# Kernel optimization log

Measured on AMD Instinct MI355X. Metric: run time of the kernel, lower is better.

## Reference

```python
import jax, jax.numpy as jnp
import numpy as np

HIDDEN = 2048
N_HEADS = 16
N_KV = 8
HEAD_DIM = HIDDEN // N_HEADS  # 128
EPS = 1e-6


def rms_norm(x, w, eps=EPS):
    xf = x.astype(jnp.float32)
    var = jnp.mean(xf * xf, axis=-1, keepdims=True)
    return (w * (xf * jax.lax.rsqrt(var + eps)).astype(x.dtype))


def rotate_half(x):
    x1, x2 = jnp.split(x, 2, axis=-1)
    return jnp.concatenate([-x2, x1], axis=-1)


def setup_inputs() -> dict:
    key = jax.random.key(0)
    ks = jax.random.split(key, 8)
    B, S = 2, 2048
    inp = {
        "hidden_states": jax.random.normal(ks[0], (B, S, HIDDEN), jnp.float32),
        "cos": jax.random.uniform(ks[1], (B, S, HEAD_DIM), jnp.float32, -1.0, 1.0),
        "sin": jax.random.uniform(ks[2], (B, S, HEAD_DIM), jnp.float32, -1.0, 1.0),
        "Wq": jax.random.normal(ks[3], (N_HEADS * HEAD_DIM, HIDDEN), jnp.float32) * 0.02,
        "Wk": jax.random.normal(ks[4], (N_KV * HEAD_DIM, HIDDEN), jnp.float32) * 0.02,
        "Wv": jax.random.normal(ks[5], (N_KV * HEAD_DIM, HIDDEN), jnp.float32) * 0.02,
        "Wo": jax.random.normal(ks[6], (HIDDEN, N_HEADS * HEAD_DIM), jnp.float32) * 0.02,
        "q_norm_w": jnp.ones((HEAD_DIM,), jnp.float32),
        "k_norm_w": jnp.ones((HEAD_DIM,), jnp.float32),
    }
    return inp


def reference(hidden_states, cos, sin, Wq, Wk, Wv, Wo, q_norm_w, k_norm_w):
    B, S, _ = hidden_states.shape
    scale = HEAD_DIM ** -0.5
    n_rep = N_HEADS // N_KV

    q = (hidden_states @ Wq.T).reshape(B, S, N_HEADS, HEAD_DIM)
    k = (hidden_states @ Wk.T).reshape(B, S, N_KV, HEAD_DIM)
    v = (hidden_states @ Wv.T).reshape(B, S, N_KV, HEAD_DIM)

    q = rms_norm(q, q_norm_w)
    k = rms_norm(k, k_norm_w)

    # -> (B, H, S, D)
    q = q.transpose(0, 2, 1, 3)
    k = k.transpose(0, 2, 1, 3)
    v = v.transpose(0, 2, 1, 3)

    c = cos[:, None, :, :]  # (B,1,S,D)
    s = sin[:, None, :, :]
    q = q * c + rotate_half(q) * s
    k = k * c + rotate_half(k) * s

    k = jnp.repeat(k, n_rep, axis=1)
    v = jnp.repeat(v, n_rep, axis=1)

    scores = jnp.einsum("bhqd,bhkd->bhqk", q, k) * scale
    attn = jax.nn.softmax(scores.astype(jnp.float32), axis=-1).astype(hidden_states.dtype)
    out = jnp.einsum("bhqk,bhkd->bhqd", attn, v)
    out = out.transpose(0, 2, 1, 3).reshape(B, S, N_HEADS * HEAD_DIM)
    return out @ Wo.T
```

## Files before the change

### kernel.cpp

```cpp
#include <hip/hip_runtime.h>
#include <cstdint>

#define SEQ 2048
#define BATCH 2
#define TOK 4096
#define HID 2048
#define NH 16
#define NKV 8
#define HD 128
#define QKV_LD 4096

using f16x8 = __attribute__((ext_vector_type(8))) _Float16;
using f32x4 = __attribute__((ext_vector_type(4))) float;

#define MFMA(a, b, c) __builtin_amdgcn_mfma_f32_16x16x32_f16(a, b, c, 0, 0, 0)

__device__ inline void gload16(const void* g, void* l) {
    __builtin_amdgcn_global_load_lds(
        (const __attribute__((address_space(1))) unsigned*)g,
        (__attribute__((address_space(3))) unsigned*)l, 16, 0, 0);
}

__device__ inline float exp2_fast(float x) {
#if __has_builtin(__builtin_amdgcn_exp2f)
    return __builtin_amdgcn_exp2f(x);
#else
    float r;
    asm("v_exp_f32 %0, %1\n\ts_nop 1" : "=v"(r) : "v"(x));
    return r;
#endif
}

__global__ __launch_bounds__(256) void conv_all(
    const float* __restrict__ hidden, const float* __restrict__ Wq,
    const float* __restrict__ Wk, const float* __restrict__ Wv,
    const float* __restrict__ Wo, _Float16* __restrict__ HhG,
    _Float16* __restrict__ WallH, _Float16* __restrict__ WoH)
{
    const int bid = blockIdx.x;
    const float* src;
    _Float16* dst;
    int row;
    if (bid < 4096)      { row = bid;        src = hidden; dst = HhG; }
    else if (bid < 6144) { row = bid - 4096; src = Wq;     dst = WallH; }
    else if (bid < 7168) { row = bid - 6144; src = Wk;     dst = WallH + (size_t)2048 * HID; }
    else if (bid < 8192) { row = bid - 7168; src = Wv;     dst = WallH + (size_t)3072 * HID; }
    else                 { row = bid - 8192; src = Wo;     dst = WoH; }

    const int gch = threadIdx.x;
    const float* s = src + (size_t)row * HID + gch * 8;
    float4 a = *(const float4*)s;
    float4 b = *(const float4*)(s + 4);
    f16x8 v;
    v[0] = (_Float16)a.x; v[1] = (_Float16)a.y;
    v[2] = (_Float16)a.z; v[3] = (_Float16)a.w;
    v[4] = (_Float16)b.x; v[5] = (_Float16)b.y;
    v[6] = (_Float16)b.z; v[7] = (_Float16)b.w;
    *(f16x8*)((char*)dst + (size_t)row * 4096 + gch * 16) = v;
}

template<bool HALF_OUT>
__global__ __launch_bounds__(512, 2) void gemm256(
    const _Float16* __restrict__ Ag, const _Float16* __restrict__ Bg,
    void* __restrict__ Cv, int ldc, int K)
{
    __shared__ char lds[2][4][16384];

    const int tid = threadIdx.x;
    const int wv = tid >> 6, ln = tid & 63;
    const int wm = wv >> 2, wn = wv & 3;
    const int lr = ln & 15, lq = ln >> 4;
    const int bn = blockIdx.x, bm = blockIdx.y;

    f32x4 acc[8][4] = {};

    const size_t arow0 = (size_t)bm * 256;
    const size_t brow0 = (size_t)bn * 256;

    const int g = tid & 7;
    uint32_t offA[2][2], offB[2][2];
#pragma unroll
    for (int i = 0; i < 2; ++i) {
        const int row = (i * 512 + tid) >> 3;
        const uint32_t sw = (uint32_t)((g ^ (row & 7)) << 4);
        offA[0][i] = (uint32_t)((arow0 + row) * 4096) + sw;
        offA[1][i] = (uint32_t)((arow0 + 128 + row) * 4096) + sw;
        offB[0][i] = (uint32_t)((brow0 + row) * 4096) + sw;
        offB[1][i] = (uint32_t)((brow0 + 128 + row) * 4096) + sw;
    }
    const int dst0 = wv * 64 * 16;

    const int swz0 = ((lq ^ (lr & 7)) << 4);
    const int swz1 = (((4 + lq) ^ (lr & 7)) << 4);

#define STAGE_ALL(bufsel, t)                                                   \
    { _Pragma("unroll")                                                        \
      for (int i = 0; i < 2; ++i) {                                            \
        gload16((const char*)Ag + offA[0][i] + (size_t)(t) * 128,              \
                &lds[bufsel][0][i * 8192 + dst0]);                             \
        gload16((const char*)Ag + offA[1][i] + (size_t)(t) * 128,              \
                &lds[bufsel][1][i * 8192 + dst0]);                             \
        gload16((const char*)Bg + offB[0][i] + (size_t)(t) * 128,              \
                &lds[bufsel][2][i * 8192 + dst0]);                             \
        gload16((const char*)Bg + offB[1][i] + (size_t)(t) * 128,              \
                &lds[bufsel][3][i * 8192 + dst0]);                             \
      } }

    STAGE_ALL(0, 0);
    asm volatile("s_waitcnt vmcnt(0)" ::: "memory");
    __builtin_amdgcn_s_barrier();

    const int NT = K / 64;
    for (int t = 0; t < NT; ++t) {
        const int buf = t & 1;
        const char* Ab = &lds[buf][wm][0];
        const char* Bb = &lds[buf][2 + (wn >> 1)][(wn & 1) * 64 * 128];

        f16x8 bfr[4][2];
#pragma unroll
        for (int nj = 0; nj < 4; ++nj) {
            bfr[nj][0] = *(const f16x8*)(Bb + (nj * 16 + lr) * 128 + swz0);
            bfr[nj][1] = *(const f16x8*)(Bb + (nj * 16 + lr) * 128 + swz1);
        }

        if (t + 1 < NT) STAGE_ALL(buf ^ 1, t + 1);

        __builtin_amdgcn_s_setprio(1);
#pragma unroll
        for (int mi = 0; mi < 8; ++mi) {
            f16x8 a0 = *(const f16x8*)(Ab + (mi * 16 + lr) * 128 + swz0);
            f16x8 a1 = *(const f16x8*)(Ab + (mi * 16 + lr) * 128 + swz1);
#pragma unroll
            for (int nj = 0; nj < 4; ++nj) {
                acc[mi][nj] = MFMA(a0, bfr[nj][0], acc[mi][nj]);
                acc[mi][nj] = MFMA(a1, bfr[nj][1], acc[mi][nj]);
            }
        }
        __builtin_amdgcn_s_setprio(0);

        asm volatile("s_waitcnt vmcnt(0)" ::: "memory");
        __builtin_amdgcn_s_barrier();
    }
#undef STAGE_ALL

#pragma unroll
    for (int mi = 0; mi < 8; ++mi)
#pragma unroll
        for (int r = 0; r < 4; ++r) {
            const size_t rowoff =
                (size_t)(arow0 + wm * 128 + mi * 16 + lq * 4 + r) * ldc
                + brow0 + wn * 64 + lr;
            if constexpr (HALF_OUT) {
                _Float16* rowp = (_Float16*)Cv + rowoff;
#pragma unroll
                for (int nj = 0; nj < 4; ++nj)
                    rowp[nj * 16] = (_Float16)acc[mi][nj][r];
            } else {
                float* rowp = (float*)Cv + rowoff;
#pragma unroll
                for (int nj = 0; nj < 4; ++nj)
                    rowp[nj * 16] = acc[mi][nj][r];
            }
        }
}

__global__ __launch_bounds__(512, 1) void gemm256x128(
    const _Float16* __restrict__ Ag, const _Float16* __restrict__ Bg,
    float* __restrict__ C, int ldc, int K)
{
    __shared__ char lds[2][3][16384];

    const int tid = threadIdx.x;
    const int wv = tid >> 6, ln = tid & 63;
    const int wm = wv >> 1, wn = wv & 1;
    const int lr = ln & 15, lq = ln >> 4;
    const int bn = blockIdx.x, bm = blockIdx.y;

    f32x4 acc[4][4] = {};

    const size_t arow0 = (size_t)bm * 256;
    const size_t brow0 = (size_t)bn * 128;

    const int g = tid & 7;
    uint32_t offA[2][2], offB[2];
#pragma unroll
    for (int i = 0; i < 2; ++i) {
        const int row = (i * 512 + tid) >> 3;
        const uint32_t sw = (uint32_t)((g ^ (row & 7)) << 4);
        offA[0][i] = (uint32_t)((arow0 + row) * 4096) + sw;
        offA[1][i] = (uint32_t)((arow0 + 128 + row) * 4096) + sw;
        offB[i]    = (uint32_t)((brow0 + row) * 4096) + sw;
    }
    const int dst0 = wv * 64 * 16;

    const int swz0 = ((lq ^ (lr & 7)) << 4);
    const int swz1 = (((4 + lq) ^ (lr & 7)) << 4);

#define STAGE_ALL2(bufsel, t)                                                  \
    { _Pragma("unroll")                                                        \
      for (int i = 0; i < 2; ++i) {                                            \
        gload16((const char*)Ag + offA[0][i] + (size_t)(t) * 128,              \
                &lds[bufsel][0][i * 8192 + dst0]);                             \
        gload16((const char*)Ag + offA[1][i] + (size_t)(t) * 128,              \
                &lds[bufsel][1][i * 8192 + dst0]);                             \
        gload16((const char*)Bg + offB[i] + (size_t)(t) * 128,                 \
                &lds[bufsel][2][i * 8192 + dst0]);                             \
      } }

    STAGE_ALL2(0, 0);
    asm volatile("s_waitcnt vmcnt(0)" ::: "memory");
    __builtin_amdgcn_s_barrier();

    const int NT = K / 64;
    for (int t = 0; t < NT; ++t) {
        const int buf = t & 1;
        const char* Ab = &lds[buf][wm >> 1][(wm & 1) * 64 * 128];
        const char* Bb = &lds[buf][2][wn * 64 * 128];

        f16x8 bfr[4][2];
#pragma unroll
        for (int nj = 0; nj < 4; ++nj) {
            bfr[nj][0] = *(const f16x8*)(Bb + (nj * 16 + lr) * 128 + swz0);
            bfr[nj][1] = *(const f16x8*)(Bb + (nj * 16 + lr) * 128 + swz1);
        }

        if (t + 1 < NT) STAGE_ALL2(buf ^ 1, t + 1);

        __builtin_amdgcn_s_setprio(1);
#pragma unroll
        for (int mi = 0; mi < 4; ++mi) {
            f16x8 a0 = *(const f16x8*)(Ab + (mi * 16 + lr) * 128 + swz0);
            f16x8 a1 = *(const f16x8*)(Ab + (mi * 16 + lr) * 128 + swz1);
#pragma unroll
            for (int nj = 0; nj < 4; ++nj) {
                acc[mi][nj] = MFMA(a0, bfr[nj][0], acc[mi][nj]);
                acc[mi][nj] = MFMA(a1, bfr[nj][1], acc[mi][nj]);
            }
        }
        __builtin_amdgcn_s_setprio(0);

        asm volatile("s_waitcnt vmcnt(0)" ::: "memory");
        __builtin_amdgcn_s_barrier();
    }
#undef STAGE_ALL2

#pragma unroll
    for (int mi = 0; mi < 4; ++mi)
#pragma unroll
        for (int r = 0; r < 4; ++r) {
            float* rowp = C + (size_t)(arow0 + wm * 64 + mi * 16 + lq * 4 + r) * ldc
                          + brow0 + wn * 64 + lr;
#pragma unroll
            for (int nj = 0; nj < 4; ++nj)
                rowp[nj * 16] = acc[mi][nj][r];
        }
}

__global__ __launch_bounds__(256) void norm_rope(
    const _Float16* __restrict__ P, const float* __restrict__ cosb,
    const float* __restrict__ sinb, const float* __restrict__ qw,
    const float* __restrict__ kw, _Float16* __restrict__ QhG,
    _Float16* __restrict__ KhG)
{
    const int t    = blockIdx.y;
    const int wave = threadIdx.x >> 6;
    const int lane = threadIdx.x & 63;
    const int hid  = blockIdx.x * 4 + wave;
    const float QS = 0.08838834764831845f * 1.4426950408889634f;

    const _Float16* ptr;
    const float* w;
    if (hid < NH) { ptr = P + (size_t)t * QKV_LD + hid * HD;              w = qw; }
    else          { ptr = P + (size_t)t * QKV_LD + HID + (hid - NH) * HD; w = kw; }

    float x1 = (float)ptr[lane];
    float x2 = (float)ptr[lane + 64];
    float ss = x1 * x1 + x2 * x2;
#pragma unroll
    for (int off = 1; off < 64; off <<= 1) ss += __shfl_xor(ss, off);
    const float r = rsqrtf(ss * (1.f / 128.f) + 1e-6f);
    const float n1 = x1 * r * w[lane];
    const float n2 = x2 * r * w[lane + 64];

    const float* cp = cosb + (size_t)t * HD;
    const float* sp = sinb + (size_t)t * HD;
    const float o1 = n1 * cp[lane]      - n2 * sp[lane];
    const float o2 = n2 * cp[lane + 64] + n1 * sp[lane + 64];

    if (hid < NH) {
        _Float16* qrow = QhG + (size_t)t * HID + hid * HD;
        qrow[lane]      = (_Float16)(o1 * QS);
        qrow[lane + 64] = (_Float16)(o2 * QS);
    } else {
        const int b = t / SEQ, s = t % SEQ, kv = hid - NH;
        char* ph = (char*)KhG + ((size_t)(b * NKV + kv) * SEQ + s) * 256;
        const int s7 = s & 7;
        const int d1 = lane, d2 = lane + 64;
        *(_Float16*)(ph + (((d1 >> 3) ^ s7) << 4) + ((d1 & 7) << 1)) = (_Float16)o1;
        *(_Float16*)(ph + (((d2 >> 3) ^ s7) << 4) + ((d2 & 7) << 1)) = (_Float16)o2;
    }
}

__global__ __launch_bounds__(256) void conv_v(
    const _Float16* __restrict__ P, _Float16* __restrict__ VtG)
{
    __shared__ _Float16 Ts[64][136];
    const int kb = blockIdx.x;
    const int kv = blockIdx.y;
    const int tid = threadIdx.x;

#pragma unroll
    for (int r = 0; r < 4; ++r) {
        const int idx = tid + r * 256;
        const int row = idx >> 4, c8 = idx & 15;
        *(f16x8*)&Ts[row][c8 * 8] =
            *(const f16x8*)(P + (size_t)(kb * 64 + row) * QKV_LD
                            + HID + NKV * HD + kv * HD + c8 * 8);
    }
    __syncthreads();

    const int b  = (kb * 64) / SEQ;
    const int s0 = (kb * 64) % SEQ;
#pragma unroll
    for (int w = 0; w < 4; ++w) {
        const int idx = tid + w * 256;
        const int d = idx >> 3, c = idx & 7;
        f16x8 pk;
#pragma unroll
        for (int kk = 0; kk < 8; ++kk) pk[kk] = Ts[c * 8 + kk][d];
        char* dst = (char*)VtG + ((size_t)(b * NKV + kv) * 128 + d) * 4096
                    + ((s0 >> 3) + (c ^ (d & 7))) * 16;
        *(f16x8*)dst = pk;
    }
}

__global__ __launch_bounds__(256, 2) void flash_f16(
    const _Float16* __restrict__ QhG, const _Float16* __restrict__ KhG,
    const _Float16* __restrict__ VtG, _Float16* __restrict__ OH)
{
    __shared__ char KhL[2][16384];
    __shared__ char VtL[16384];
    __shared__ _Float16 Pl[4][32][72];

    const int id  = blockIdx.x + 16 * (blockIdx.y + 16 * blockIdx.z);
    const int swz = (id & 7) * 64 + (id >> 3);
    const int qt = swz & 15, h = (swz >> 4) & 15, b = swz >> 8;

    const int hkv = h >> 1;
    const int tid = threadIdx.x, wv = tid >> 6, ln = tid & 63;
    const int lr = ln & 15, lq = ln >> 4;
    const int qbase = qt * 128 + wv * 32;
    const float BIAS = 3.0f * 1.4426950408889634f;

    f16x8 qh[2][4];
#pragma unroll
    for (int mi = 0; mi < 2; ++mi)
#pragma unroll
        for (int kc = 0; kc < 4; ++kc)
            qh[mi][kc] = *(const f16x8*)(QhG
                + (size_t)(b * SEQ + qbase + mi * 16 + lr) * HID
                + h * HD + kc * 32 + lq * 8);

    f32x4 o_[2][8] = {};
    float rs[2][4] = {};

    const size_t krow = (size_t)(b * NKV + hkv) * SEQ;
    const size_t vrow = (size_t)(b * NKV + hkv) * 128;

    const char* kg[4];
    const char* vg[4];
    int dofs[4];
#pragma unroll
    for (int r = 0; r < 4; ++r) {
        const int idx = tid + r * 256;
        kg[r] = (const char*)KhG + (krow + (idx >> 4)) * 256 + (idx & 15) * 16;
        vg[r] = (const char*)VtG + (vrow + (idx >> 3)) * 4096 + (idx & 7) * 16;
        dofs[r] = (r * 256 + wv * 64) * 16;
    }

#define STAGE_K(buf, kt)                                                      \
    { _Pragma("unroll")                                                       \
      for (int r = 0; r < 4; ++r)                                             \
          gload16(kg[r] + (size_t)(kt) * 16384, &KhL[buf][dofs[r]]); }
#define STAGE_V(kt)                                                           \
    { _Pragma("unroll")                                                       \
      for (int r = 0; r < 4; ++r)                                             \
          gload16(vg[r] + (kt) * 128, &VtL[dofs[r]]); }

    STAGE_K(0, 0);
    STAGE_V(0);
    STAGE_K(1, 1);
    __syncthreads();

    const int NT = SEQ / 64;
    for (int kt = 0; kt < NT; ++kt) {
        const int buf = kt & 1;

        f32x4 s[2][4];
        __builtin_amdgcn_s_setprio(1);
#pragma unroll
        for (int nt = 0; nt < 4; ++nt) {
            const int key = nt * 16 + lr;
            f16x8 kh[4];
#pragma unroll
            for (int kc = 0; kc < 4; ++kc)
                kh[kc] = *(f16x8*)(&KhL[buf][key * 256 +
                                   ((((kc * 4 + lq) ^ (lr & 7))) << 4)]);
#pragma unroll
            for (int mi = 0; mi < 2; ++mi) {
                f32x4 sa = {-BIAS, -BIAS, -BIAS, -BIAS};
#pragma unroll
                for (int kc = 0; kc < 4; ++kc)
                    sa = MFMA(qh[mi][kc], kh[kc], sa);
                s[mi][nt] = sa;
            }
        }
        __builtin_amdgcn_s_setprio(0);

#pragma unroll
        for (int mi = 0; mi < 2; ++mi)
#pragma unroll
            for (int nt = 0; nt < 4; ++nt)
#pragma unroll
                for (int r = 0; r < 4; ++r) {
                    const float p = exp2_fast(s[mi][nt][r]);
                    rs[mi][r] += p;
                    Pl[wv][mi * 16 + lq * 4 + r][nt * 16 + lr] = (_Float16)p;
                }
        f16x8 pa[2][2];
#pragma unroll
        for (int mi = 0; mi < 2; ++mi) {
            pa[mi][0] = *(f16x8*)&Pl[wv][mi * 16 + lr][lq * 8];
            pa[mi][1] = *(f16x8*)&Pl[wv][mi * 16 + lr][32 + lq * 8];
        }

        if (kt + 1 < NT) {
            asm volatile("s_waitcnt vmcnt(4)" ::: "memory");
        } else {
            asm volatile("s_waitcnt vmcnt(0)" ::: "memory");
        }
        __builtin_amdgcn_s_barrier();

        __builtin_amdgcn_s_setprio(1);
#pragma unroll
        for (int nt2 = 0; nt2 < 8; ++nt2) {
            const int d0 = nt2 * 16 + lr;
            f16x8 v0 = *(f16x8*)(&VtL[d0 * 128 + ((lq ^ (d0 & 7)) << 4)]);
            f16x8 v1 = *(f16x8*)(&VtL[d0 * 128 + (((4 + lq) ^ (d0 & 7)) << 4)]);
#pragma unroll
            for (int mi = 0; mi < 2; ++mi) {
                o_[mi][nt2] = MFMA(pa[mi][0], v0, o_[mi][nt2]);
                o_[mi][nt2] = MFMA(pa[mi][1], v1, o_[mi][nt2]);
            }
        }
        __builtin_amdgcn_s_setprio(0);

        __syncthreads();

        if (kt + 1 < NT) STAGE_V(kt + 1);
        if (kt + 2 < NT) STAGE_K(buf, kt + 2);
    }

    float inv[2][4];
#pragma unroll
    for (int mi = 0; mi < 2; ++mi)
#pragma unroll
        for (int r = 0; r < 4; ++r) {
            float v = rs[mi][r];
            v += __shfl_xor(v, 1);
            v += __shfl_xor(v, 2);
            v += __shfl_xor(v, 4);
            v += __shfl_xor(v, 8);
            inv[mi][r] = 1.0f / v;
        }

#pragma unroll
    for (int mi = 0; mi < 2; ++mi)
#pragma unroll
        for (int r = 0; r < 4; ++r) {
            const int R = b * SEQ + qbase + mi * 16 + lq * 4 + r;
            _Float16* rowp = OH + (size_t)R * HID + h * HD + lr;
#pragma unroll
            for (int nt2 = 0; nt2 < 8; ++nt2)
                rowp[nt2 * 16] = (_Float16)(o_[mi][nt2][r] * inv[mi][r]);
        }
#undef STAGE_K
#undef STAGE_V
}

extern "C" void kernel_launch(void* const* d_in, const int* in_sizes, int n_in,
                              void* d_out, int out_size, void* d_ws, size_t ws_size,
                              hipStream_t stream)
{
    (void)in_sizes; (void)n_in; (void)out_size; (void)ws_size;
    const float* hidden = (const float*)d_in[0];
    const float* cosb   = (const float*)d_in[1];
    const float* sinb   = (const float*)d_in[2];
    const float* Wq     = (const float*)d_in[3];
    const float* Wk     = (const float*)d_in[4];
    const float* Wv     = (const float*)d_in[5];
    const float* Wo     = (const float*)d_in[6];
    const float* qw     = (const float*)d_in[7];
    const float* kw     = (const float*)d_in[8];
    float* out = (float*)d_out;

    char* ws = (char*)d_ws;
    const size_t MB = 1ull << 20;
    _Float16*  P16   = (_Float16*)(ws);
    _Float16*  attnH = (_Float16*)(ws + 32  * MB);
    _Float16*  HhG   = (_Float16*)(ws + 48  * MB);
    _Float16*  WallH = (_Float16*)(ws + 64  * MB);
    _Float16*  WoH   = (_Float16*)(ws + 80  * MB);
    _Float16*  KhG   = (_Float16*)(ws + 88  * MB);
    _Float16*  VtG   = (_Float16*)(ws + 96  * MB);
    _Float16*  QhG   = (_Float16*)(ws + 104 * MB);

    const dim3 blk(256);
    conv_all<<<10240, blk, 0, stream>>>(hidden, Wq, Wk, Wv, Wo, HhG, WallH, WoH);

    gemm256<true><<<dim3(16, 16), dim3(512), 0, stream>>>(HhG, WallH, P16, QKV_LD, HID);

    norm_rope<<<dim3(6, TOK), blk, 0, stream>>>(P16, cosb, sinb, qw, kw, QhG, KhG);
    conv_v<<<dim3(TOK / 64, NKV), blk, 0, stream>>>(P16, VtG);

    flash_f16<<<dim3(SEQ / 128, NH, BATCH), blk, 0, stream>>>(QhG, KhG, VtG, attnH);

    gemm256x128<<<dim3(16, 16), dim3(512), 0, stream>>>(attnH, WoH, out, HID, HID);
}
```

Measured before the change: 215.3 us.

## Double flash-attention query tile per block and remap grid for KV-head locality

Each wave now handles 64 query rows instead of 32, so a block covers 256 queries and each K/V tile loaded into LDS is reused across twice as many rows. The grid is flattened to 256 blocks with an XCD-aware mapping that places both query heads sharing a KV head, and neighbouring query tiles, on the same XCD for L2 reuse. K and V fragments are hoisted into registers before the MFMA loops. The cost is much higher register pressure (launch bounds lowered to 1 block per SM), fewer blocks in total, and lower occupancy for hiding latency.

```diff
diff --git a/kernel.cpp b/kernel.cpp
--- a/kernel.cpp
+++ b/kernel.cpp
@@ -334,35 +334,38 @@
     }
 }
 
-__global__ __launch_bounds__(256, 2) void flash_f16(
+__global__ __launch_bounds__(256, 1) void flash_f16(
     const _Float16* __restrict__ QhG, const _Float16* __restrict__ KhG,
     const _Float16* __restrict__ VtG, _Float16* __restrict__ OH)
 {
     __shared__ char KhL[2][16384];
     __shared__ char VtL[16384];
-    __shared__ _Float16 Pl[4][32][72];
-
-    const int id  = blockIdx.x + 16 * (blockIdx.y + 16 * blockIdx.z);
-    const int swz = (id & 7) * 64 + (id >> 3);
-    const int qt = swz & 15, h = (swz >> 4) & 15, b = swz >> 8;
-
-    const int hkv = h >> 1;
+    __shared__ _Float16 Pl[4][64][72];
+
+    const int raw = blockIdx.x;
+    const int xcd = raw & 7, slot = raw >> 3;
+    const int panel = xcd * 2 + (slot >> 4);
+    const int j = slot & 15;
+    const int b = panel >> 3, hkv = panel & 7;
+    const int h = hkv * 2 + (j & 1);
+    const int qt = j >> 1;
+
     const int tid = threadIdx.x, wv = tid >> 6, ln = tid & 63;
     const int lr = ln & 15, lq = ln >> 4;
-    const int qbase = qt * 128 + wv * 32;
+    const int qbase = qt * 256 + wv * 64;
     const float BIAS = 3.0f * 1.4426950408889634f;
 
-    f16x8 qh[2][4];
-#pragma unroll
-    for (int mi = 0; mi < 2; ++mi)
+    f16x8 qh[4][4];
+#pragma unroll
+    for (int mi = 0; mi < 4; ++mi)
 #pragma unroll
         for (int kc = 0; kc < 4; ++kc)
             qh[mi][kc] = *(const f16x8*)(QhG
                 + (size_t)(b * SEQ + qbase + mi * 16 + lr) * HID
                 + h * HD + kc * 32 + lq * 8);
 
-    f32x4 o_[2][8] = {};
-    float rs[2][4] = {};
+    f32x4 o_[4][8] = {};
+    float rs[4][4] = {};
 
     const size_t krow = (size_t)(b * NKV + hkv) * SEQ;
     const size_t vrow = (size_t)(b * NKV + hkv) * 128;
@@ -396,43 +399,36 @@
     for (int kt = 0; kt < NT; ++kt) {
         const int buf = kt & 1;
 
-        f32x4 s[2][4];
+        f16x8 kh[4][4];
+#pragma unroll
+        for (int nt = 0; nt < 4; ++nt)
+#pragma unroll
+            for (int kc = 0; kc < 4; ++kc)
+                kh[nt][kc] = *(f16x8*)(&KhL[buf][(nt * 16 + lr) * 256 +
+                                       ((((kc * 4 + lq) ^ (lr & 7))) << 4)]);
+
         __builtin_amdgcn_s_setprio(1);
 #pragma unroll
-        for (int nt = 0; nt < 4; ++nt) {
-            const int key = nt * 16 + lr;
-            f16x8 kh[4];
-#pragma unroll
-            for (int kc = 0; kc < 4; ++kc)
-                kh[kc] = *(f16x8*)(&KhL[buf][key * 256 +
-                                   ((((kc * 4 + lq) ^ (lr & 7))) << 4)]);
-#pragma unroll
-            for (int mi = 0; mi < 2; ++mi) {
+        for (int mi = 0; mi < 4; ++mi) {
+            f32x4 s[4];
+#pragma unroll
+            for (int nt = 0; nt < 4; ++nt) {
                 f32x4 sa = {-BIAS, -BIAS, -BIAS, -BIAS};
 #pragma unroll
                 for (int kc = 0; kc < 4; ++kc)
-                    sa = MFMA(qh[mi][kc], kh[kc], sa);
-                s[mi][nt] = sa;
+                    sa = MFMA(qh[mi][kc], kh[nt][kc], sa);
+                s[nt] = sa;
             }
-        }
-        __builtin_amdgcn_s_setprio(0);
-
-#pragma unroll
-        for (int mi = 0; mi < 2; ++mi)
 #pragma unroll
             for (int nt = 0; nt < 4; ++nt)
 #pragma unroll
                 for (int r = 0; r < 4; ++r) {
-                    const float p = exp2_fast(s[mi][nt][r]);
+                    const float p = exp2_fast(s[nt][r]);
                     rs[mi][r] += p;
                     Pl[wv][mi * 16 + lq * 4 + r][nt * 16 + lr] = (_Float16)p;
                 }
-        f16x8 pa[2][2];
-#pragma unroll
-        for (int mi = 0; mi < 2; ++mi) {
-            pa[mi][0] = *(f16x8*)&Pl[wv][mi * 16 + lr][lq * 8];
-            pa[mi][1] = *(f16x8*)&Pl[wv][mi * 16 + lr][32 + lq * 8];
-        }
+        }
+        __builtin_amdgcn_s_setprio(0);
 
         if (kt + 1 < NT) {
             asm volatile("s_waitcnt vmcnt(4)" ::: "memory");
@@ -441,18 +437,28 @@
         }
         __builtin_amdgcn_s_barrier();
 
-        __builtin_amdgcn_s_setprio(1);
+        f16x8 vf[8][2];
 #pragma unroll
         for (int nt2 = 0; nt2 < 8; ++nt2) {
             const int d0 = nt2 * 16 + lr;
-            f16x8 v0 = *(f16x8*)(&VtL[d0 * 128 + ((lq ^ (d0 & 7)) << 4)]);
-            f16x8 v1 = *(f16x8*)(&VtL[d0 * 128 + (((4 + lq) ^ (d0 & 7)) << 4)]);
-#pragma unroll
-            for (int mi = 0; mi < 2; ++mi) {
-                o_[mi][nt2] = MFMA(pa[mi][0], v0, o_[mi][nt2]);
-                o_[mi][nt2] = MFMA(pa[mi][1], v1, o_[mi][nt2]);
+            vf[nt2][0] = *(f16x8*)(&VtL[d0 * 128 + ((lq ^ (d0 & 7)) << 4)]);
+            vf[nt2][1] = *(f16x8*)(&VtL[d0 * 128 + (((4 + lq) ^ (d0 & 7)) << 4)]);
+        }
+        f16x8 pa[4][2];
+#pragma unroll
+        for (int mi = 0; mi < 4; ++mi) {
+            pa[mi][0] = *(f16x8*)&Pl[wv][mi * 16 + lr][lq * 8];
+            pa[mi][1] = *(f16x8*)&Pl[wv][mi * 16 + lr][32 + lq * 8];
+        }
+
+        __builtin_amdgcn_s_setprio(1);
+#pragma unroll
+        for (int nt2 = 0; nt2 < 8; ++nt2)
+#pragma unroll
+            for (int mi = 0; mi < 4; ++mi) {
+                o_[mi][nt2] = MFMA(pa[mi][0], vf[nt2][0], o_[mi][nt2]);
+                o_[mi][nt2] = MFMA(pa[mi][1], vf[nt2][1], o_[mi][nt2]);
             }
-        }
         __builtin_amdgcn_s_setprio(0);
 
         __syncthreads();
@@ -461,9 +467,9 @@
         if (kt + 2 < NT) STAGE_K(buf, kt + 2);
     }
 
-    float inv[2][4];
-#pragma unroll
-    for (int mi = 0; mi < 2; ++mi)
+    float inv[4][4];
+#pragma unroll
+    for (int mi = 0; mi < 4; ++mi)
 #pragma unroll
         for (int r = 0; r < 4; ++r) {
             float v = rs[mi][r];
@@ -475,7 +481,7 @@
         }
 
 #pragma unroll
-    for (int mi = 0; mi < 2; ++mi)
+    for (int mi = 0; mi < 4; ++mi)
 #pragma unroll
         for (int r = 0; r < 4; ++r) {
             const int R = b * SEQ + qbase + mi * 16 + lq * 4 + r;
@@ -523,7 +529,7 @@
     norm_rope<<<dim3(6, TOK), blk, 0, stream>>>(P16, cosb, sinb, qw, kw, QhG, KhG);
     conv_v<<<dim3(TOK / 64, NKV), blk, 0, stream>>>(P16, VtG);
 
-    flash_f16<<<dim3(SEQ / 128, NH, BATCH), blk, 0, stream>>>(QhG, KhG, VtG, attnH);
+    flash_f16<<<dim3(256), blk, 0, stream>>>(QhG, KhG, VtG, attnH);
 
     gemm256x128<<<dim3(16, 16), dim3(512), 0, stream>>>(attnH, WoH, out, HID, HID);
 }
```

After: 229.6 us. +6.7%, slower.
